# Performance work log

Hardware: AMD Instinct MI355X
Metric: run time of the kernel (lower is better)

## Reference

```python
import jax, jax.numpy as jnp
import numpy as np

ITER_STEPS = 2
NODE_DIM = 512

def _rmv(t, m, value):
    # allennlp.replace_masked_values: keep t where mask nonzero, else value
    return jnp.where(m != 0, t, value)

def setup_inputs() -> dict:
    key = jax.random.key(0)
    ks = jax.random.split(key, 24)
    B, R, C, D, d = 16, 64, 64, 2048, NODE_DIM
    inp = {
        "question_node": jax.random.normal(ks[0], (B, d), jnp.float32),
        "table_row_header_nodes": jax.random.normal(ks[1], (B, R, d), jnp.float32),
        "table_col_header_nodes": jax.random.normal(ks[2], (B, C, d), jnp.float32),
        "table_data_cell_nodes": jax.random.normal(ks[3], (B, D, d), jnp.float32),
        "table_row_header_index_mask": jax.random.randint(ks[4], (B, R), 0, 2, jnp.int32),
        "table_col_header_index_mask": jax.random.randint(ks[5], (B, C), 0, 2, jnp.int32),
        "table_data_cell_index_mask": jax.random.randint(ks[6], (B, D), 0, 2, jnp.int32),
        "same_row_data_cell_relation": jax.random.randint(ks[7], (B, D, D), 0, 2, jnp.int32),
        "same_col_data_cell_relation": jax.random.randint(ks[8], (B, D, D), 0, 2, jnp.int32),
        "data_cell_row_rel": jax.random.randint(ks[9], (B, R, D), 0, 2, jnp.int32),
        "data_cell_col_rel": jax.random.randint(ks[10], (B, C, D), 0, 2, jnp.int32),
        # parameters (Linear(in,out) stores weight [out,in]; y = x @ W.T)
        "w_node": jax.random.normal(ks[11], (1, d), jnp.float32) / np.sqrt(d),
        "w_row_data_cell": jax.random.normal(ks[12], (d, d), jnp.float32) / np.sqrt(d),
        "w_col_data_cell": jax.random.normal(ks[13], (d, d), jnp.float32) / np.sqrt(d),
        "w_data_cell_row": jax.random.normal(ks[14], (d, d), jnp.float32) / np.sqrt(d),
        "w_data_cell_col": jax.random.normal(ks[15], (d, d), jnp.float32) / np.sqrt(d),
        "w_same_row": jax.random.normal(ks[16], (d, d), jnp.float32) / np.sqrt(d),
        "w_same_col": jax.random.normal(ks[17], (d, d), jnp.float32) / np.sqrt(d),
        "w_row_question": jax.random.normal(ks[18], (d, d), jnp.float32) / np.sqrt(d),
        "w_col_question": jax.random.normal(ks[19], (d, d), jnp.float32) / np.sqrt(d),
    }
    return inp


def reference(question_node, table_row_header_nodes, table_col_header_nodes,
              table_data_cell_nodes, table_row_header_index_mask,
              table_col_header_index_mask, table_data_cell_index_mask,
              same_row_data_cell_relation, same_col_data_cell_relation,
              data_cell_row_rel, data_cell_col_rel,
              w_node, w_row_data_cell, w_col_data_cell, w_data_cell_row,
              w_data_cell_col, w_same_row, w_same_col, w_row_question,
              w_col_question):
    rm = table_row_header_index_mask.astype(jnp.float32)   # [B,R]
    cm = table_col_header_index_mask.astype(jnp.float32)   # [B,C]
    dm = table_data_cell_index_mask.astype(jnp.float32)    # [B,D]

    # masked relation graphs (0/1 float)
    rh_dc_graph = data_cell_row_rel.astype(jnp.float32) * (rm[:, :, None] * dm[:, None, :])   # [B,R,D]
    ch_dc_graph = data_cell_col_rel.astype(jnp.float32) * (cm[:, :, None] * dm[:, None, :])   # [B,C,D]
    dc_dc_mask = dm[:, :, None] * dm[:, None, :]
    same_row_graph = same_row_data_cell_relation.astype(jnp.float32) * dc_dc_mask             # [B,D,D]
    same_col_graph = same_col_data_cell_relation.astype(jnp.float32) * dc_dc_mask             # [B,D,D]

    rh_num = rh_dc_graph.sum(-1)                                  # [B,R]
    rh_num = _rmv(rh_num + 1.0, (rh_num >= 1), 1.0)
    ch_num = ch_dc_graph.sum(-1)                                  # [B,C]
    ch_num = _rmv(ch_num + 1.0, (ch_num >= 1), 1.0)
    dc_num = (same_row_graph.sum(-1) + same_col_graph.sum(-1)
              + rh_dc_graph.sum(1) + ch_dc_graph.sum(1))          # [B,D]
    dc_num = _rmv(dc_num, (dc_num >= 1), 1.0)

    rh = table_row_header_nodes
    ch = table_col_header_nodes
    dc = table_data_cell_nodes
    q = question_node

    for _ in range(ITER_STEPS):
        rh_w = jax.nn.sigmoid(rh @ w_node.T)[..., 0]   # [B,R]
        ch_w = jax.nn.sigmoid(ch @ w_node.T)[..., 0]   # [B,C]
        dc_w = jax.nn.sigmoid(dc @ w_node.T)[..., 0]   # [B,D]

        rh_dc_info = dc @ w_row_data_cell.T            # [B,D,d]
        ch_dc_info = dc @ w_col_data_cell.T            # [B,D,d]
        rh_q_info = (q @ w_row_question.T)[:, None, :] * rm[:, :, None]  # [B,R,d]
        ch_q_info = (q @ w_col_question.T)[:, None, :] * cm[:, :, None]  # [B,C,d]
        same_row_info = dc @ w_same_row.T              # [B,D,d]
        same_col_info = dc @ w_same_col.T              # [B,D,d]
        dc_rh_info = rh @ w_data_cell_row.T            # [B,R,d]
        dc_ch_info = ch @ w_data_cell_col.T            # [B,C,d]

        # gated adjacency weights: source-node sigmoid gate masked by graph
        rh_dc_weight = jnp.where(rh_dc_graph != 0, dc_w[:, None, :], 0.0)         # [B,R,D]
        ch_dc_weight = jnp.where(ch_dc_graph != 0, dc_w[:, None, :], 0.0)         # [B,C,D]
        same_row_weight = jnp.where(same_row_graph != 0, dc_w[:, None, :], 0.0)   # [B,D,D]
        same_col_weight = jnp.where(same_col_graph != 0, dc_w[:, None, :], 0.0)   # [B,D,D]
        dc_rh_weight = jnp.where(jnp.swapaxes(rh_dc_graph, 1, 2) != 0, rh_w[:, None, :], 0.0)  # [B,D,R]
        dc_ch_weight = jnp.where(jnp.swapaxes(ch_dc_graph, 1, 2) != 0, ch_w[:, None, :], 0.0)  # [B,D,C]

        rh_dc_agg = jnp.matmul(rh_dc_weight, rh_dc_info)        # [B,R,d]
        ch_dc_agg = jnp.matmul(ch_dc_weight, ch_dc_info)        # [B,C,d]
        same_row_agg = jnp.matmul(same_row_weight, same_row_info)  # [B,D,d]
        same_col_agg = jnp.matmul(same_col_weight, same_col_info)  # [B,D,d]
        dc_rh_agg = jnp.matmul(dc_rh_weight, dc_rh_info)        # [B,D,d]
        dc_ch_agg = jnp.matmul(dc_ch_weight, dc_ch_info)        # [B,D,d]

        agg_rh = (rh_dc_agg + rh_q_info) / rh_num[:, :, None]
        agg_ch = (ch_dc_agg + ch_q_info) / ch_num[:, :, None]
        # NOTE: faithful to source bug: dc_ch_agg appears twice, same_col_agg unused
        agg_dc = (same_row_agg + dc_ch_agg + dc_rh_agg + dc_ch_agg) / dc_num[:, :, None]

        rh = jax.nn.relu(agg_rh)
        ch = jax.nn.relu(agg_ch)
        dc = jax.nn.relu(agg_dc)

    return (rh, ch, dc)
```

## Files before the change

### kernel.cpp

```cpp
#include <hip/hip_runtime.h>
#include <math.h>

#define NB 16
#define NR 64
#define NCOL 64
#define ND 2048
#define DIM 512

typedef __attribute__((ext_vector_type(4))) float f32x4;
typedef __attribute__((ext_vector_type(8))) short bf16x8;
typedef __attribute__((ext_vector_type(8))) unsigned short us8;

#define OFF_RHNUM  0L
#define OFF_CHNUM  1024L
#define OFF_DCNUM  2048L
#define OFF_RHW    34816L
#define OFF_CHW    35840L
#define OFF_QROW   36864L
#define OFF_QCOL   45056L
#define OFF_PRER   53248L
#define OFF_PREC   577536L
#define OFF_INFORC 1101824L
#define OFF_BITS   2150400L
#define OFF_DCS    4247552L
#define OFF_PROJ   21024768L
#define WS_FLOATS  37801984L

__device__ inline void bsplit(float v, unsigned short& h, unsigned short& l) {
    unsigned uv = __float_as_uint(v);
    unsigned hb = (uv + 0x7FFFu + ((uv >> 16) & 1u)) >> 16;
    h = (unsigned short)hb;
    float lo = v - __uint_as_float(hb << 16);
    unsigned lv = __float_as_uint(lo);
    l = (unsigned short)((lv + 0x7FFFu + ((lv >> 16) & 1u)) >> 16);
}

__global__ __launch_bounds__(256) void k_gate_rc(
    const float* __restrict__ rh, const float* __restrict__ ch,
    const int* __restrict__ rm, const int* __restrict__ cm,
    const float* __restrict__ wnode,
    float* __restrict__ rh_w, float* __restrict__ ch_w)
{
    int wave = threadIdx.x >> 6, lane = threadIdx.x & 63;
    int idx = blockIdx.x * 4 + wave;
    const float* xrow; float* outw; int mval;
    if (idx < NB * NR) {
        int b = idx >> 6, r = idx & 63;
        xrow = rh + ((long)b * NR + r) * DIM; mval = rm[b * NR + r]; outw = rh_w + b * NR + r;
    } else {
        int tt = idx - NB * NR; int b = tt >> 6, c = tt & 63;
        xrow = ch + ((long)b * NCOL + c) * DIM; mval = cm[b * NCOL + c]; outw = ch_w + b * NCOL + c;
    }
    const float4* px = (const float4*)xrow;
    const float4* pw = (const float4*)wnode;
    float4 xa = px[lane * 2], xb = px[lane * 2 + 1];
    float4 wa = pw[lane * 2], wb = pw[lane * 2 + 1];
    float s = xa.x * wa.x + xa.y * wa.y + xa.z * wa.z + xa.w * wa.w
            + xb.x * wb.x + xb.y * wb.y + xb.z * wb.z + xb.w * wb.w;
    #pragma unroll
    for (int o = 32; o > 0; o >>= 1) s += __shfl_xor(s, o, 64);
    if (lane == 0) {
        float g = 1.f / (1.f + expf(-s));
        *outw = mval ? g : 0.f;
    }
}

__global__ __launch_bounds__(256) void k_split(
    const float* __restrict__ src, const float* __restrict__ wnode, const int* __restrict__ dmask,
    unsigned short* __restrict__ dhi, unsigned short* __restrict__ dlo)
{
    int wave = threadIdx.x >> 6, lane = threadIdx.x & 63;
    long idx = (long)blockIdx.x * 4 + wave;
    const float* row = src + idx * DIM;
    const float4* px = (const float4*)row;
    const float4* pw = (const float4*)wnode;
    float4 xa = px[lane * 2], xb = px[lane * 2 + 1];
    float4 wa = pw[lane * 2], wb = pw[lane * 2 + 1];
    float s = xa.x * wa.x + xa.y * wa.y + xa.z * wa.z + xa.w * wa.w
            + xb.x * wb.x + xb.y * wb.y + xb.z * wb.z + xb.w * wb.w;
    #pragma unroll
    for (int o = 32; o > 0; o >>= 1) s += __shfl_xor(s, o, 64);
    float g = 1.f / (1.f + expf(-s));
    float sc = (dmask[idx] != 0) ? g : 0.f;
    float v[8] = {sc * xa.x, sc * xa.y, sc * xa.z, sc * xa.w,
                  sc * xb.x, sc * xb.y, sc * xb.z, sc * xb.w};
    us8 ph, pl;
    #pragma unroll
    for (int i = 0; i < 8; i++) {
        unsigned short hh, ll; bsplit(v[i], hh, ll);
        ph[i] = hh; pl[i] = ll;
    }
    *(us8*)(dhi + idx * DIM + lane * 8) = ph;
    *(us8*)(dlo + idx * DIM + lane * 8) = pl;
}

__global__ __launch_bounds__(256) void k_wsplit(
    const float* __restrict__ w, unsigned short* __restrict__ whi, unsigned short* __restrict__ wlo)
{
    long i = ((long)blockIdx.x * 256 + threadIdx.x) * 8;
    float4 a = *(const float4*)(w + i), b4 = *(const float4*)(w + i + 4);
    float v[8] = {a.x, a.y, a.z, a.w, b4.x, b4.y, b4.z, b4.w};
    us8 ph, pl;
    #pragma unroll
    for (int t = 0; t < 8; t++) {
        unsigned short hh, ll; bsplit(v[t], hh, ll);
        ph[t] = hh; pl[t] = ll;
    }
    *(us8*)(whi + i) = ph;
    *(us8*)(wlo + i) = pl;
}

__global__ __launch_bounds__(256) void k_q(
    const float* __restrict__ q, const float* __restrict__ wrq, const float* __restrict__ wcq,
    float* __restrict__ qrow, float* __restrict__ qcol)
{
    int b = blockIdx.z;
    const float* W = blockIdx.y ? wcq : wrq;
    float* out = blockIdx.y ? qcol : qrow;
    int wave = threadIdx.x >> 6, lane = threadIdx.x & 63;
    int n = blockIdx.x * 4 + wave;
    const float4* qp = (const float4*)(q + (long)b * DIM);
    const float4* wp = (const float4*)(W + (long)n * DIM);
    float4 a0 = qp[lane * 2], a1 = qp[lane * 2 + 1];
    float4 w0 = wp[lane * 2], w1 = wp[lane * 2 + 1];
    float s = a0.x * w0.x + a0.y * w0.y + a0.z * w0.z + a0.w * w0.w
            + a1.x * w1.x + a1.y * w1.y + a1.z * w1.z + a1.w * w1.w;
    #pragma unroll
    for (int o = 32; o > 0; o >>= 1) s += __shfl_xor(s, o, 64);
    if (lane == 0) out[(long)b * DIM + n] = s;
}

__global__ __launch_bounds__(256) void k_bits(
    const int* __restrict__ sr, const int* __restrict__ sc, const int* __restrict__ dmask,
    unsigned* __restrict__ bits, float* __restrict__ dcnum)
{
    long bi = blockIdx.x;
    int b = (int)(bi >> 11);
    const int* dmb = dmask + (long)b * ND;
    int dmi = dmb[bi & 2047];
    int wave = threadIdx.x >> 6, lane = threadIdx.x & 63;
    const int* srrow = sr + bi * ND;
    const int* scrow = sc + bi * ND;
    unsigned* brow = bits + bi * 64;
    int cnt = 0;
    for (int rr = 0; rr < 8; rr++) {
        int j = wave * 512 + rr * 64 + lane;
        int dmj = dmb[j] != 0;
        bool p1 = dmi && dmj && (srrow[j] != 0);
        unsigned long long m1 = __ballot(p1);
        bool p2 = dmi && dmj && (scrow[j] != 0);
        unsigned long long m2 = __ballot(p2);
        if (lane == 0) {
            int w0 = wave * 16 + rr * 2;
            brow[w0] = (unsigned)m1; brow[w0 + 1] = (unsigned)(m1 >> 32);
        }
        cnt += __popcll(m1) + __popcll(m2);
    }
    __shared__ int red[4];
    if (lane == 0) red[wave] = cnt;
    __syncthreads();
    if (threadIdx.x == 0) dcnum[bi] = (float)(red[0] + red[1] + red[2] + red[3]);
}

__global__ __launch_bounds__(256) void k_rcnum(
    const int* __restrict__ rel_rd, const int* __restrict__ rel_cd,
    const int* __restrict__ rm, const int* __restrict__ cm, const int* __restrict__ dmask,
    float* __restrict__ rh_num, float* __restrict__ ch_num)
{
    int wave = threadIdx.x >> 6, lane = threadIdx.x & 63;
    long idx = (long)blockIdx.x * 4 + wave;
    const int* row; int mval; float* out; const int* dmb;
    if (idx < NB * NR) {
        int b = (int)(idx >> 6), r = (int)(idx & 63);
        row = rel_rd + ((long)b * NR + r) * ND; mval = rm[b * NR + r];
        out = rh_num + b * NR + r; dmb = dmask + (long)b * ND;
    } else {
        long tt = idx - NB * NR; int b = (int)(tt >> 6), c = (int)(tt & 63);
        row = rel_cd + ((long)b * NCOL + c) * ND; mval = cm[b * NCOL + c];
        out = ch_num + b * NCOL + c; dmb = dmask + (long)b * ND;
    }
    int cnt = 0;
    for (int rr = 0; rr < 32; rr++) {
        int j = rr * 64 + lane;
        cnt += (row[j] != 0 && dmb[j] != 0) ? 1 : 0;
    }
    #pragma unroll
    for (int o = 32; o > 0; o >>= 1) cnt += __shfl_xor(cnt, o, 64);
    if (lane == 0) {
        float s = mval ? (float)cnt : 0.f;
        *out = (s >= 1.f) ? (s + 1.f) : 1.f;
    }
}

__global__ __launch_bounds__(256) void k_dcnum_final(
    const int* __restrict__ rel_rd, const int* __restrict__ rel_cd,
    const int* __restrict__ rm, const int* __restrict__ cm, const int* __restrict__ dmask,
    float* __restrict__ dcnum)
{
    int b = blockIdx.y;
    int j = blockIdx.x * 256 + threadIdx.x;
    const int* rd = rel_rd + (long)b * NR * ND;
    const int* cd = rel_cd + (long)b * NCOL * ND;
    const int* rmb = rm + b * NR;
    const int* cmb = cm + b * NCOL;
    int cnt = 0;
    for (int r = 0; r < NR; r++)  cnt += (rd[(long)r * ND + j] != 0 && rmb[r] != 0) ? 1 : 0;
    for (int c = 0; c < NCOL; c++) cnt += (cd[(long)c * ND + j] != 0 && cmb[c] != 0) ? 1 : 0;
    float add = (dmask[(long)b * ND + j] != 0) ? (float)cnt : 0.f;
    float tv = dcnum[(long)b * ND + j] + add;
    dcnum[(long)b * ND + j] = (tv >= 1.f) ? tv : 1.f;
}

template<int EPI>
__global__ __launch_bounds__(256) void gemm_small(
    const float* __restrict__ A, long sA,
    const float* __restrict__ W,
    float* __restrict__ C, long sC,
    const float* __restrict__ rowscale, float alpha,
    const int* __restrict__ mrow, const float* __restrict__ addvec,
    const float* __restrict__ rownum, int rsb)
{
    int b = blockIdx.z;
    int n0 = blockIdx.x * 64;
    __shared__ float As[32][68], Ws[32][68];
    float acc[4][4] = {};
    int tx = threadIdx.x & 15, ty = threadIdx.x >> 4;
    int lm = threadIdx.x >> 2, lk = (threadIdx.x & 3) * 8;
    const float* Ab = A + (long)b * sA;
    for (int k0 = 0; k0 < DIM; k0 += 32) {
        const float4* pa = (const float4*)(Ab + (long)lm * DIM + k0 + lk);
        float4 va0 = pa[0], va1 = pa[1];
        const float4* pw = (const float4*)(W + (long)(n0 + lm) * DIM + k0 + lk);
        float4 vw0 = pw[0], vw1 = pw[1];
        As[lk + 0][lm] = va0.x; As[lk + 1][lm] = va0.y; As[lk + 2][lm] = va0.z; As[lk + 3][lm] = va0.w;
        As[lk + 4][lm] = va1.x; As[lk + 5][lm] = va1.y; As[lk + 6][lm] = va1.z; As[lk + 7][lm] = va1.w;
        Ws[lk + 0][lm] = vw0.x; Ws[lk + 1][lm] = vw0.y; Ws[lk + 2][lm] = vw0.z; Ws[lk + 3][lm] = vw0.w;
        Ws[lk + 4][lm] = vw1.x; Ws[lk + 5][lm] = vw1.y; Ws[lk + 6][lm] = vw1.z; Ws[lk + 7][lm] = vw1.w;
        __syncthreads();
        #pragma unroll
        for (int kk = 0; kk < 32; kk++) {
            float4 av = *(const float4*)&As[kk][ty * 4];
            float4 wv = *(const float4*)&Ws[kk][tx * 4];
            float a[4] = {av.x, av.y, av.z, av.w};
            float w[4] = {wv.x, wv.y, wv.z, wv.w};
            #pragma unroll
            for (int mi = 0; mi < 4; mi++)
                #pragma unroll
                for (int ni = 0; ni < 4; ni++)
                    acc[mi][ni] += a[mi] * w[ni];
        }
        __syncthreads();
    }
    #pragma unroll
    for (int mi = 0; mi < 4; mi++) {
        int gm = ty * 4 + mi;
        float vals[4];
        if (EPI == 1) {
            float scv = alpha * rowscale[(long)b * rsb + gm];
            #pragma unroll
            for (int ni = 0; ni < 4; ni++) vals[ni] = scv * acc[mi][ni];
        } else {
            float mq = (mrow[(long)b * rsb + gm] != 0) ? 1.f : 0.f;
            float inv = 1.f / rownum[(long)b * rsb + gm];
            #pragma unroll
            for (int ni = 0; ni < 4; ni++) {
                float tv = (acc[mi][ni] + mq * addvec[(long)b * DIM + n0 + tx * 4 + ni]) * inv;
                vals[ni] = fmaxf(tv, 0.f);
            }
        }
        float4 o; o.x = vals[0]; o.y = vals[1]; o.z = vals[2]; o.w = vals[3];
        *(float4*)(C + (long)b * sC + (long)gm * DIM + n0 + tx * 4) = o;
    }
}

__global__ __launch_bounds__(256) void k_proj_mfma(
    const unsigned short* __restrict__ whi, const unsigned short* __restrict__ wlo,
    const unsigned short* __restrict__ dhi, const unsigned short* __restrict__ dlo,
    unsigned short* __restrict__ phi, unsigned short* __restrict__ plo)
{
    int flat = blockIdx.x;
    int tile = (flat & 7) * 128 + (flat >> 3);
    int b = tile >> 6;
    int rem = tile & 63;
    int m0 = (rem >> 4) * 128;
    int n0 = (rem & 15) * 128;

    __shared__ unsigned short Ahi[128 * 64], Alo[128 * 64];
    __shared__ unsigned short Bhi[128 * 64], Blo[128 * 64];

    int tid = threadIdx.x;
    int lane = tid & 63, wid = tid >> 6;
    int wm = wid >> 1, wn = wid & 1;

    int srow = tid >> 1, sseg = tid & 1;

    f32x4 acc[4][4];
    #pragma unroll
    for (int i = 0; i < 4; i++)
        #pragma unroll
        for (int j = 0; j < 4; j++)
            acc[i][j] = (f32x4){0.f, 0.f, 0.f, 0.f};

    for (int k0 = 0; k0 < DIM; k0 += 64) {
        {
            const uint4* ph = (const uint4*)(whi + (long)(m0 + srow) * DIM + k0 + sseg * 32);
            const uint4* pl = (const uint4*)(wlo + (long)(m0 + srow) * DIM + k0 + sseg * 32);
            #pragma unroll
            for (int s = 0; s < 4; s++) {
                int c = (sseg * 4 + s) ^ (srow & 7);
                *(uint4*)((char*)Ahi + srow * 128 + c * 16) = ph[s];
                *(uint4*)((char*)Alo + srow * 128 + c * 16) = pl[s];
            }
        }
        {
            const uint4* ph = (const uint4*)(dhi + ((long)b * ND + n0 + srow) * DIM + k0 + sseg * 32);
            const uint4* pl = (const uint4*)(dlo + ((long)b * ND + n0 + srow) * DIM + k0 + sseg * 32);
            #pragma unroll
            for (int s = 0; s < 4; s++) {
                int c = (sseg * 4 + s) ^ (srow & 7);
                *(uint4*)((char*)Bhi + srow * 128 + c * 16) = ph[s];
                *(uint4*)((char*)Blo + srow * 128 + c * 16) = pl[s];
            }
        }
        __syncthreads();
        #pragma unroll
        for (int ks = 0; ks < 2; ks++) {
            bf16x8 ah[4], al[4], bh[4], bl[4];
            #pragma unroll
            for (int i = 0; i < 4; i++) {
                int rr = wm * 64 + i * 16 + (lane & 15);
                int cc = (ks * 4 + (lane >> 4)) ^ (rr & 7);
                ah[i] = *(bf16x8*)((char*)Ahi + rr * 128 + cc * 16);
                al[i] = *(bf16x8*)((char*)Alo + rr * 128 + cc * 16);
                int nn = wn * 64 + i * 16 + (lane & 15);
                int c2 = (ks * 4 + (lane >> 4)) ^ (nn & 7);
                bh[i] = *(bf16x8*)((char*)Bhi + nn * 128 + c2 * 16);
                bl[i] = *(bf16x8*)((char*)Blo + nn * 128 + c2 * 16);
            }
            #pragma unroll
            for (int mi = 0; mi < 4; mi++)
                #pragma unroll
                for (int ni = 0; ni < 4; ni++) {
                    acc[mi][ni] = __builtin_amdgcn_mfma_f32_16x16x32_bf16(ah[mi], bh[ni], acc[mi][ni], 0, 0, 0);
                    acc[mi][ni] = __builtin_amdgcn_mfma_f32_16x16x32_bf16(ah[mi], bl[ni], acc[mi][ni], 0, 0, 0);
                    acc[mi][ni] = __builtin_amdgcn_mfma_f32_16x16x32_bf16(al[mi], bh[ni], acc[mi][ni], 0, 0, 0);
                }
        }
        __syncthreads();
    }
    #pragma unroll
    for (int mi = 0; mi < 4; mi++) {
        int grow = m0 + wm * 64 + mi * 16 + (lane >> 4) * 4;
        #pragma unroll
        for (int ni = 0; ni < 4; ni++) {
            int gcol = n0 + wn * 64 + ni * 16 + (lane & 15);
            #pragma unroll
            for (int r = 0; r < 4; r++) {
                unsigned short hh, ll; bsplit(acc[mi][ni][r], hh, ll);
                long off = ((long)b * DIM + grow + r) * ND + gcol;
                phi[off] = hh; plo[off] = ll;
            }
        }
    }
}

__global__ __launch_bounds__(256) void k_pre_rc(
    const int* __restrict__ rel_rd, const int* __restrict__ rel_cd,
    const unsigned short* __restrict__ dhi, const unsigned short* __restrict__ dlo,
    const int* __restrict__ rm, const int* __restrict__ cm,
    float* __restrict__ pre_r, float* __restrict__ pre_c)
{
    int b = blockIdx.z, n0 = blockIdx.x * 64;
    const int* rel = blockIdx.y ? rel_cd : rel_rd;
    const int* msk = blockIdx.y ? cm : rm;
    float* outp = blockIdx.y ? pre_c : pre_r;
    __shared__ float As[64][68], Bs[64][68];
    float acc[4][4] = {};
    int tx = threadIdx.x & 15, ty = threadIdx.x >> 4;
    int am = threadIdx.x >> 2, ak = (threadIdx.x & 3) * 16;
    int bj = threadIdx.x >> 2, bseg = threadIdx.x & 3;
    for (int k0 = 0; k0 < ND; k0 += 64) {
        const int4* pa = (const int4*)(rel + ((long)b * 64 + am) * ND + k0 + ak);
        #pragma unroll
        for (int s4 = 0; s4 < 4; s4++) {
            int4 v = pa[s4];
            As[ak + s4 * 4 + 0][am] = v.x ? 1.f : 0.f;
            As[ak + s4 * 4 + 1][am] = v.y ? 1.f : 0.f;
            As[ak + s4 * 4 + 2][am] = v.z ? 1.f : 0.f;
            As[ak + s4 * 4 + 3][am] = v.w ? 1.f : 0.f;
        }
        long sb = ((long)b * ND + k0 + bj) * DIM + n0 + bseg * 16;
        us8 h0 = *(const us8*)(dhi + sb);
        us8 h1 = *(const us8*)(dhi + sb + 8);
        us8 l0 = *(const us8*)(dlo + sb);
        us8 l1 = *(const us8*)(dlo + sb + 8);
        #pragma unroll
        for (int t = 0; t < 8; t++) {
            Bs[bj][bseg * 16 + t] =
                __uint_as_float((unsigned)h0[t] << 16) + __uint_as_float((unsigned)l0[t] << 16);
            Bs[bj][bseg * 16 + 8 + t] =
                __uint_as_float((unsigned)h1[t] << 16) + __uint_as_float((unsigned)l1[t] << 16);
        }
        __syncthreads();
        #pragma unroll 8
        for (int kk = 0; kk < 64; kk++) {
            float4 av = *(const float4*)&As[kk][ty * 4];
            float4 bv = *(const float4*)&Bs[kk][tx * 4];
            float a[4] = {av.x, av.y, av.z, av.w};
            float w[4] = {bv.x, bv.y, bv.z, bv.w};
            #pragma unroll
            for (int mi = 0; mi < 4; mi++)
                #pragma unroll
                for (int ni = 0; ni < 4; ni++)
                    acc[mi][ni] += a[mi] * w[ni];
        }
        __syncthreads();
    }
    #pragma unroll
    for (int mi = 0; mi < 4; mi++) {
        int gm = ty * 4 + mi;
        float scv = (msk[b * 64 + gm] != 0) ? 1.f : 0.f;
        float4 o; o.x = scv * acc[mi][0]; o.y = scv * acc[mi][1]; o.z = scv * acc[mi][2]; o.w = scv * acc[mi][3];
        *(float4*)(outp + ((long)b * 64 + gm) * DIM + n0 + tx * 4) = o;
    }
}

__global__ __launch_bounds__(256) void k_aggdc(
    const int* __restrict__ rel_rd, const int* __restrict__ rel_cd,
    const float* __restrict__ info_rc, const int* __restrict__ dmask,
    float* __restrict__ out)
{
    int b = blockIdx.z, m0 = blockIdx.y * 128, n0 = blockIdx.x * 128;
    __shared__ float As[32][132], Bs[32][132];
    float acc[8][8] = {};
    int tx = threadIdx.x & 15, ty = threadIdx.x >> 4;
    int ak = threadIdx.x >> 3, aj = (threadIdx.x & 7) * 16;
    for (int kt = 0; kt < 4; kt++) {
        const int* rel = (kt < 2) ? rel_rd : rel_cd;
        int krow = (kt & 1) * 32 + ak;
        const int4* pa = (const int4*)(rel + ((long)b * 64 + krow) * ND + m0 + aj);
        #pragma unroll
        for (int s = 0; s < 4; s++) {
            int4 v = pa[s];
            float4 f; f.x = v.x ? 1.f : 0.f; f.y = v.y ? 1.f : 0.f; f.z = v.z ? 1.f : 0.f; f.w = v.w ? 1.f : 0.f;
            *(float4*)&As[ak][aj + s * 4] = f;
        }
        const float4* pb = (const float4*)(info_rc + ((long)b * 128 + kt * 32 + ak) * DIM + n0 + aj);
        #pragma unroll
        for (int s = 0; s < 4; s++) *(float4*)&Bs[ak][aj + s * 4] = pb[s];
        __syncthreads();
        #pragma unroll 4
        for (int kk = 0; kk < 32; kk++) {
            float4 a0 = *(const float4*)&As[kk][ty * 8];
            float4 a1 = *(const float4*)&As[kk][ty * 8 + 4];
            float4 b0 = *(const float4*)&Bs[kk][tx * 8];
            float4 b1 = *(const float4*)&Bs[kk][tx * 8 + 4];
            float a[8] = {a0.x, a0.y, a0.z, a0.w, a1.x, a1.y, a1.z, a1.w};
            float w[8] = {b0.x, b0.y, b0.z, b0.w, b1.x, b1.y, b1.z, b1.w};
            #pragma unroll
            for (int mi = 0; mi < 8; mi++)
                #pragma unroll
                for (int ni = 0; ni < 8; ni++)
                    acc[mi][ni] += a[mi] * w[ni];
        }
        __syncthreads();
    }
    #pragma unroll
    for (int mi = 0; mi < 8; mi++) {
        int gm = m0 + ty * 8 + mi;
        float mq = (dmask[(long)b * ND + gm] != 0) ? 1.f : 0.f;
        float* po = out + ((long)b * ND + gm) * DIM + n0 + tx * 8;
        float4 o0; o0.x = mq * acc[mi][0]; o0.y = mq * acc[mi][1]; o0.z = mq * acc[mi][2]; o0.w = mq * acc[mi][3];
        float4 o1; o1.x = mq * acc[mi][4]; o1.y = mq * acc[mi][5]; o1.z = mq * acc[mi][6]; o1.w = mq * acc[mi][7];
        *(float4*)(po) = o0; *(float4*)(po + 4) = o1;
    }
}

__global__ __launch_bounds__(256) void k_agg_final(
    const unsigned* __restrict__ bits,
    const unsigned short* __restrict__ phi, const unsigned short* __restrict__ plo,
    const float* __restrict__ aggdc, const float* __restrict__ rownum,
    float* __restrict__ out)
{
    int flat = blockIdx.x;
    int tile = (flat & 7) * 128 + (flat >> 3);
    int b = tile >> 6;
    int m0 = ((tile >> 2) & 15) * 128;
    int n0 = (tile & 3) * 128;

    __shared__ unsigned short Aexp[128 * 64];
    __shared__ unsigned short Bhi[128 * 64];
    __shared__ unsigned short Blo[128 * 64];

    int tid = threadIdx.x;
    int lane = tid & 63, wid = tid >> 6;
    int wm = wid >> 1, wn = wid & 1;

    int arow = tid >> 1, awsel = tid & 1;
    const unsigned* abit_base = bits + ((long)b * ND + m0 + arow) * 64 + awsel;

    f32x4 acc[4][4];
    #pragma unroll
    for (int i = 0; i < 4; i++)
        #pragma unroll
        for (int j = 0; j < 4; j++)
            acc[i][j] = (f32x4){0.f, 0.f, 0.f, 0.f};

    for (int k0 = 0; k0 < ND; k0 += 64) {
        #pragma unroll
        for (int u = 0; u < 8; u++) {
            int lin = (u & 3) * 256 + tid;
            int n = lin >> 3, c = lin & 7;
            const unsigned short* src = (u < 4 ? phi : plo)
                + ((long)b * DIM + n0 + n) * ND + k0 + c * 8;
            uint4 v = *(const uint4*)src;
            char* dst = (char*)(u < 4 ? Bhi : Blo) + n * 128 + ((c ^ (n & 7)) * 16);
            *(uint4*)dst = v;
        }
        {
            unsigned w = abit_base[k0 >> 5];
            char* ab = (char*)Aexp + arow * 128;
            #pragma unroll
            for (int c = 0; c < 4; c++) {
                uint4 qv;
                qv.x = (((w >> (c * 8 + 0)) & 1u) ? 0x3F80u : 0u) | (((w >> (c * 8 + 1)) & 1u) ? 0x3F800000u : 0u);
                qv.y = (((w >> (c * 8 + 2)) & 1u) ? 0x3F80u : 0u) | (((w >> (c * 8 + 3)) & 1u) ? 0x3F800000u : 0u);
                qv.z = (((w >> (c * 8 + 4)) & 1u) ? 0x3F80u : 0u) | (((w >> (c * 8 + 5)) & 1u) ? 0x3F800000u : 0u);
                qv.w = (((w >> (c * 8 + 6)) & 1u) ? 0x3F80u : 0u) | (((w >> (c * 8 + 7)) & 1u) ? 0x3F800000u : 0u);
                int chunk = (awsel * 4 + c) ^ (arow & 7);
                *(uint4*)(ab + chunk * 16) = qv;
            }
        }
        __syncthreads();
        #pragma unroll
        for (int ks = 0; ks < 2; ks++) {
            bf16x8 af[4], bh[4], bl[4];
            #pragma unroll
            for (int i = 0; i < 4; i++) {
                int rr = wm * 64 + i * 16 + (lane & 15);
                int cc = (ks * 4 + (lane >> 4)) ^ (rr & 7);
                af[i] = *(bf16x8*)((char*)Aexp + rr * 128 + cc * 16);
                int nn = wn * 64 + i * 16 + (lane & 15);
                int c2 = (ks * 4 + (lane >> 4)) ^ (nn & 7);
                bh[i] = *(bf16x8*)((char*)Bhi + nn * 128 + c2 * 16);
                bl[i] = *(bf16x8*)((char*)Blo + nn * 128 + c2 * 16);
            }
            #pragma unroll
            for (int mi = 0; mi < 4; mi++)
                #pragma unroll
                for (int ni = 0; ni < 4; ni++) {
                    acc[mi][ni] = __builtin_amdgcn_mfma_f32_16x16x32_bf16(af[mi], bh[ni], acc[mi][ni], 0, 0, 0);
                    acc[mi][ni] = __builtin_amdgcn_mfma_f32_16x16x32_bf16(af[mi], bl[ni], acc[mi][ni], 0, 0, 0);
                }
        }
        __syncthreads();
    }
    #pragma unroll
    for (int mi = 0; mi < 4; mi++) {
        int grow = m0 + wm * 64 + mi * 16 + (lane >> 4) * 4;
        float inv[4];
        #pragma unroll
        for (int r = 0; r < 4; r++) inv[r] = 1.f / rownum[(long)b * ND + grow + r];
        #pragma unroll
        for (int ni = 0; ni < 4; ni++) {
            int gcol = n0 + wn * 64 + ni * 16 + (lane & 15);
            #pragma unroll
            for (int r = 0; r < 4; r++) {
                long off = ((long)b * ND + grow + r) * DIM + gcol;
                out[off] = fmaxf((acc[mi][ni][r] + aggdc[off]) * inv[r], 0.f);
            }
        }
    }
}

extern "C" void kernel_launch(void* const* d_in, const int* in_sizes, int n_in,
                              void* d_out, int out_size, void* d_ws, size_t ws_size,
                              hipStream_t stream)
{
    const float* q       = (const float*)d_in[0];
    const float* rh0     = (const float*)d_in[1];
    const float* ch0     = (const float*)d_in[2];
    const float* dc0     = (const float*)d_in[3];
    const int*   rm      = (const int*)d_in[4];
    const int*   cm      = (const int*)d_in[5];
    const int*   dmask   = (const int*)d_in[6];
    const int*   same_row= (const int*)d_in[7];
    const int*   same_col= (const int*)d_in[8];
    const int*   rel_rd  = (const int*)d_in[9];
    const int*   rel_cd  = (const int*)d_in[10];
    const float* wnode   = (const float*)d_in[11];
    const float* w_rdc   = (const float*)d_in[12];
    const float* w_cdc   = (const float*)d_in[13];
    const float* w_dcr   = (const float*)d_in[14];
    const float* w_dcc   = (const float*)d_in[15];
    const float* w_sr    = (const float*)d_in[16];
    const float* w_rq    = (const float*)d_in[18];
    const float* w_cq    = (const float*)d_in[19];

    float* out = (float*)d_out;
    float* rh = out;
    float* ch = out + (long)NB * NR * DIM;
    float* dc = out + (long)NB * NR * DIM * 2;

    if (ws_size < (size_t)WS_FLOATS * 4) return;

    float* ws      = (float*)d_ws;
    float* rh_num  = ws + OFF_RHNUM;
    float* ch_num  = ws + OFF_CHNUM;
    float* dc_num  = ws + OFF_DCNUM;
    float* rh_w    = ws + OFF_RHW;
    float* ch_w    = ws + OFF_CHW;
    float* qrow    = ws + OFF_QROW;
    float* qcol    = ws + OFF_QCOL;
    float* pre_r   = ws + OFF_PRER;
    float* pre_c   = ws + OFF_PREC;
    float* info_rc = ws + OFF_INFORC;
    unsigned* bits = (unsigned*)(ws + OFF_BITS);
    unsigned short* dhi = (unsigned short*)(ws + OFF_DCS);
    unsigned short* dlo = dhi + (size_t)NB * ND * DIM;
    unsigned short* phi = (unsigned short*)(ws + OFF_PROJ);
    unsigned short* plo = phi + (size_t)NB * DIM * ND;
    float* aggdc   = ws + OFF_DCS;
    unsigned short* whi = (unsigned short*)(ws + OFF_PRER);
    unsigned short* wlo = whi + (size_t)DIM * DIM;

    hipMemcpyAsync(rh, rh0, sizeof(float) * (size_t)NB * NR * DIM, hipMemcpyDeviceToDevice, stream);
    hipMemcpyAsync(ch, ch0, sizeof(float) * (size_t)NB * NCOL * DIM, hipMemcpyDeviceToDevice, stream);

    k_bits<<<NB * ND, 256, 0, stream>>>(same_row, same_col, dmask, bits, dc_num);
    k_rcnum<<<512, 256, 0, stream>>>(rel_rd, rel_cd, rm, cm, dmask, rh_num, ch_num);
    k_dcnum_final<<<dim3(ND / 256, NB), 256, 0, stream>>>(rel_rd, rel_cd, rm, cm, dmask, dc_num);
    k_q<<<dim3(128, 2, NB), 256, 0, stream>>>(q, w_rq, w_cq, qrow, qcol);

    for (int it = 0; it < 2; it++) {
        k_gate_rc<<<512, 256, 0, stream>>>(rh, ch, rm, cm, wnode, rh_w, ch_w);
        k_split<<<8192, 256, 0, stream>>>(it == 0 ? dc0 : dc, wnode, dmask, dhi, dlo);
        k_wsplit<<<128, 256, 0, stream>>>(w_sr, whi, wlo);
        gemm_small<1><<<dim3(8, 1, NB), 256, 0, stream>>>(rh, (long)NR * DIM, w_dcr,
            info_rc, 128L * DIM, rh_w, 1.0f, nullptr, nullptr, nullptr, NR);
        gemm_small<1><<<dim3(8, 1, NB), 256, 0, stream>>>(ch, (long)NCOL * DIM, w_dcc,
            info_rc + 64L * DIM, 128L * DIM, ch_w, 2.0f, nullptr, nullptr, nullptr, NCOL);
        k_proj_mfma<<<1024, 256, 0, stream>>>(whi, wlo, dhi, dlo, phi, plo);
        k_pre_rc<<<dim3(8, 2, NB), 256, 0, stream>>>(rel_rd, rel_cd, dhi, dlo, rm, cm, pre_r, pre_c);
        k_aggdc<<<dim3(4, 16, NB), 256, 0, stream>>>(rel_rd, rel_cd, info_rc, dmask, aggdc);
        gemm_small<2><<<dim3(8, 1, NB), 256, 0, stream>>>(pre_r, (long)NR * DIM, w_rdc,
            rh, (long)NR * DIM, nullptr, 1.0f, rm, qrow, rh_num, NR);
        gemm_small<2><<<dim3(8, 1, NB), 256, 0, stream>>>(pre_c, (long)NCOL * DIM, w_cdc,
            ch, (long)NCOL * DIM, nullptr, 1.0f, cm, qcol, ch_num, NCOL);
        k_agg_final<<<1024, 256, 0, stream>>>(bits, phi, plo, aggdc, dc_num, dc);
    }
}
```

Measured before the change: 1.157 ms.

## Move row/col pre-aggregation to bf16 MFMA using transposed split data cells

k_split now stages 16 data-cell rows in shared memory and, besides the row-major hi/lo bf16 split, writes a transposed hi/lo copy so that a new MFMA kernel can compute the rel_rd/rel_cd times data-cell products with bf16 matrix instructions instead of the FP32 scalar tile GEMM. The transposed buffers reuse the projection workspace, so the pre-aggregation is moved ahead of k_proj_mfma, and the split weights now live in the dc output buffer. k_bits is also rewritten to use vectorised int4 loads and bit interleaving. The cost is extra transposed writes in k_split and a changed bit layout that the consumer must match.

New measurement: 1.147 ms. No clear change (-0.8%).

```diff
diff --git a/kernel.cpp b/kernel.cpp
--- a/kernel.cpp
+++ b/kernel.cpp
@@ -35,6 +35,13 @@
     l = (unsigned short)((lv + 0x7FFFu + ((lv >> 16) & 1u)) >> 16);
 }
 
+__device__ inline unsigned spread4(unsigned x) {
+    x = (x | (x << 12)) & 0x000F000Fu;
+    x = (x | (x << 6))  & 0x03030303u;
+    x = (x | (x << 3))  & 0x11111111u;
+    return x;
+}
+
 __global__ __launch_bounds__(256) void k_gate_rc(
     const float* __restrict__ rh, const float* __restrict__ ch,
     const int* __restrict__ rm, const int* __restrict__ cm,
@@ -67,31 +74,65 @@
 
 __global__ __launch_bounds__(256) void k_split(
     const float* __restrict__ src, const float* __restrict__ wnode, const int* __restrict__ dmask,
-    unsigned short* __restrict__ dhi, unsigned short* __restrict__ dlo)
-{
-    int wave = threadIdx.x >> 6, lane = threadIdx.x & 63;
-    long idx = (long)blockIdx.x * 4 + wave;
-    const float* row = src + idx * DIM;
-    const float4* px = (const float4*)row;
-    const float4* pw = (const float4*)wnode;
-    float4 xa = px[lane * 2], xb = px[lane * 2 + 1];
-    float4 wa = pw[lane * 2], wb = pw[lane * 2 + 1];
-    float s = xa.x * wa.x + xa.y * wa.y + xa.z * wa.z + xa.w * wa.w
-            + xb.x * wb.x + xb.y * wb.y + xb.z * wb.z + xb.w * wb.w;
-    #pragma unroll
-    for (int o = 32; o > 0; o >>= 1) s += __shfl_xor(s, o, 64);
-    float g = 1.f / (1.f + expf(-s));
-    float sc = (dmask[idx] != 0) ? g : 0.f;
-    float v[8] = {sc * xa.x, sc * xa.y, sc * xa.z, sc * xa.w,
-                  sc * xb.x, sc * xb.y, sc * xb.z, sc * xb.w};
-    us8 ph, pl;
+    unsigned short* __restrict__ dhi, unsigned short* __restrict__ dlo,
+    unsigned short* __restrict__ thi, unsigned short* __restrict__ tlo)
+{
+    int b = blockIdx.y, j0 = blockIdx.x * 16;
+    __shared__ float X[16 * 512];
+    __shared__ float scs[16];
+    int t = threadIdx.x;
+    int r = t >> 4, u = t & 15;
+    const float* row = src + ((long)b * ND + j0 + r) * DIM;
+    float part = 0.f;
     #pragma unroll
     for (int i = 0; i < 8; i++) {
-        unsigned short hh, ll; bsplit(v[i], hh, ll);
-        ph[i] = hh; pl[i] = ll;
-    }
-    *(us8*)(dhi + idx * DIM + lane * 8) = ph;
-    *(us8*)(dlo + idx * DIM + lane * 8) = pl;
+        int col = i * 64 + u * 4;
+        float4 v = *(const float4*)(row + col);
+        float4 w = *(const float4*)(wnode + col);
+        part += v.x * w.x + v.y * w.y + v.z * w.z + v.w * w.w;
+        *(float4*)&X[r * 512 + (col ^ ((r & 7) * 4))] = v;
+    }
+    part += __shfl_xor(part, 1, 64);
+    part += __shfl_xor(part, 2, 64);
+    part += __shfl_xor(part, 4, 64);
+    part += __shfl_xor(part, 8, 64);
+    if (u == 0) {
+        float g = 1.f / (1.f + expf(-part));
+        scs[r] = (dmask[(long)b * ND + j0 + r] != 0) ? g : 0.f;
+    }
+    __syncthreads();
+    {
+        float s = scs[r];
+        long ob = ((long)b * ND + j0 + r) * DIM + u * 32;
+        #pragma unroll
+        for (int g = 0; g < 4; g++) {
+            us8 ph, pl;
+            #pragma unroll
+            for (int e = 0; e < 8; e++) {
+                int cc = u * 32 + g * 8 + e;
+                float v = X[r * 512 + (cc ^ ((r & 7) * 4))] * s;
+                unsigned short hh, ll; bsplit(v, hh, ll);
+                ph[e] = hh; pl[e] = ll;
+            }
+            *(us8*)(dhi + ob + g * 8) = ph;
+            *(us8*)(dlo + ob + g * 8) = pl;
+        }
+    }
+    #pragma unroll
+    for (int h = 0; h < 2; h++) {
+        int n = t + h * 256;
+        us8 ph0, ph1, pl0, pl1;
+        #pragma unroll
+        for (int rr = 0; rr < 16; rr++) {
+            float v = X[rr * 512 + (n ^ ((rr & 7) * 4))] * scs[rr];
+            unsigned short hh, ll; bsplit(v, hh, ll);
+            if (rr < 8) { ph0[rr] = hh; pl0[rr] = ll; }
+            else        { ph1[rr - 8] = hh; pl1[rr - 8] = ll; }
+        }
+        long ob = ((long)b * DIM + n) * ND + j0;
+        *(us8*)(thi + ob) = ph0; *(us8*)(thi + ob + 8) = ph1;
+        *(us8*)(tlo + ob) = pl0; *(us8*)(tlo + ob + 8) = pl1;
+    }
 }
 
 __global__ __launch_bounds__(256) void k_wsplit(
@@ -136,25 +177,37 @@
 {
     long bi = blockIdx.x;
     int b = (int)(bi >> 11);
-    const int* dmb = dmask + (long)b * ND;
-    int dmi = dmb[bi & 2047];
+    int dmi = dmask[bi];
     int wave = threadIdx.x >> 6, lane = threadIdx.x & 63;
-    const int* srrow = sr + bi * ND;
-    const int* scrow = sc + bi * ND;
+    const int4* sr4 = (const int4*)(sr + bi * ND);
+    const int4* sc4 = (const int4*)(sc + bi * ND);
+    const int4* dm4 = (const int4*)(dmask + (long)b * ND);
     unsigned* brow = bits + bi * 64;
     int cnt = 0;
-    for (int rr = 0; rr < 8; rr++) {
-        int j = wave * 512 + rr * 64 + lane;
-        int dmj = dmb[j] != 0;
-        bool p1 = dmi && dmj && (srrow[j] != 0);
-        unsigned long long m1 = __ballot(p1);
-        bool p2 = dmi && dmj && (scrow[j] != 0);
-        unsigned long long m2 = __ballot(p2);
-        if (lane == 0) {
-            int w0 = wave * 16 + rr * 2;
-            brow[w0] = (unsigned)m1; brow[w0 + 1] = (unsigned)(m1 >> 32);
-        }
-        cnt += __popcll(m1) + __popcll(m2);
+    #pragma unroll
+    for (int h = 0; h < 2; h++) {
+        int vidx = wave * 128 + h * 64 + lane;
+        int4 vs = sr4[vidx];
+        int4 vc = sc4[vidx];
+        int4 vd = dm4[vidx];
+        bool d0 = dmi && vd.x, d1 = dmi && vd.y, d2 = dmi && vd.z, d3 = dmi && vd.w;
+        unsigned long long m0 = __ballot(d0 && vs.x);
+        unsigned long long m1 = __ballot(d1 && vs.y);
+        unsigned long long m2 = __ballot(d2 && vs.z);
+        unsigned long long m3 = __ballot(d3 && vs.w);
+        unsigned long long n0 = __ballot(d0 && vc.x);
+        unsigned long long n1 = __ballot(d1 && vc.y);
+        unsigned long long n2 = __ballot(d2 && vc.z);
+        unsigned long long n3 = __ballot(d3 && vc.w);
+        cnt += __popcll(m0) + __popcll(m1) + __popcll(m2) + __popcll(m3)
+             + __popcll(n0) + __popcll(n1) + __popcll(n2) + __popcll(n3);
+        if (lane < 8) {
+            unsigned w = spread4((unsigned)(m0 >> (8 * lane)) & 0xFFu)
+                       | (spread4((unsigned)(m1 >> (8 * lane)) & 0xFFu) << 1)
+                       | (spread4((unsigned)(m2 >> (8 * lane)) & 0xFFu) << 2)
+                       | (spread4((unsigned)(m3 >> (8 * lane)) & 0xFFu) << 3);
+            brow[wave * 16 + h * 8 + lane] = w;
+        }
     }
     __shared__ int red[4];
     if (lane == 0) red[wave] = cnt;
@@ -273,6 +326,102 @@
     }
 }
 
+__global__ __launch_bounds__(256) void k_pre_rc_mfma(
+    const int* __restrict__ rel_rd, const int* __restrict__ rel_cd,
+    const unsigned short* __restrict__ thi, const unsigned short* __restrict__ tlo,
+    const int* __restrict__ rm, const int* __restrict__ cm,
+    float* __restrict__ pre_r, float* __restrict__ pre_c)
+{
+    int b = blockIdx.y, n0 = blockIdx.x * 64;
+    __shared__ unsigned short Aexp[128 * 64];
+    __shared__ unsigned short Bhi[64 * 64], Blo[64 * 64];
+    int tid = threadIdx.x, lane = tid & 63, wid = tid >> 6;
+    int wm = wid >> 1, wn = wid & 1;
+    int arow = tid >> 1, aseg = tid & 1;
+    const int* relrow = (arow < 64)
+        ? rel_rd + ((long)b * 64 + arow) * ND
+        : rel_cd + ((long)b * 64 + arow - 64) * ND;
+    int bn = tid >> 2, bq = tid & 3;
+    const unsigned short* bsrc_h = thi + ((long)b * DIM + n0 + bn) * ND;
+    const unsigned short* bsrc_l = tlo + ((long)b * DIM + n0 + bn) * ND;
+
+    f32x4 acc[4][2];
+    #pragma unroll
+    for (int i = 0; i < 4; i++)
+        #pragma unroll
+        for (int j = 0; j < 2; j++)
+            acc[i][j] = (f32x4){0.f, 0.f, 0.f, 0.f};
+
+    for (int k0 = 0; k0 < ND; k0 += 64) {
+        {
+            const int4* pa = (const int4*)(relrow + k0 + aseg * 32);
+            #pragma unroll
+            for (int p = 0; p < 4; p++) {
+                int4 v0 = pa[2 * p], v1 = pa[2 * p + 1];
+                uint4 qv;
+                qv.x = (v0.x ? 0x3F80u : 0u) | (v0.y ? 0x3F800000u : 0u);
+                qv.y = (v0.z ? 0x3F80u : 0u) | (v0.w ? 0x3F800000u : 0u);
+                qv.z = (v1.x ? 0x3F80u : 0u) | (v1.y ? 0x3F800000u : 0u);
+                qv.w = (v1.z ? 0x3F80u : 0u) | (v1.w ? 0x3F800000u : 0u);
+                int c = (aseg * 4 + p) ^ (arow & 7);
+                *(uint4*)((char*)Aexp + arow * 128 + c * 16) = qv;
+            }
+        }
+        {
+            const uint4* ph = (const uint4*)(bsrc_h + k0 + bq * 16);
+            const uint4* pl = (const uint4*)(bsrc_l + k0 + bq * 16);
+            #pragma unroll
+            for (int s = 0; s < 2; s++) {
+                int c = (bq * 2 + s) ^ (bn & 7);
+                *(uint4*)((char*)Bhi + bn * 128 + c * 16) = ph[s];
+                *(uint4*)((char*)Blo + bn * 128 + c * 16) = pl[s];
+            }
+        }
+        __syncthreads();
+        #pragma unroll
+        for (int ks = 0; ks < 2; ks++) {
+            bf16x8 af[4], bh[2], bl[2];
+            #pragma unroll
+            for (int i = 0; i < 4; i++) {
+                int rr = wm * 64 + i * 16 + (lane & 15);
+                int cc = (ks * 4 + (lane >> 4)) ^ (rr & 7);
+                af[i] = *(bf16x8*)((char*)Aexp + rr * 128 + cc * 16);
+            }
+            #pragma unroll
+            for (int i = 0; i < 2; i++) {
+                int nn = wn * 32 + i * 16 + (lane & 15);
+                int c2 = (ks * 4 + (lane >> 4)) ^ (nn & 7);
+                bh[i] = *(bf16x8*)((char*)Bhi + nn * 128 + c2 * 16);
+                bl[i] = *(bf16x8*)((char*)Blo + nn * 128 + c2 * 16);
+            }
+            #pragma unroll
+            for (int mi = 0; mi < 4; mi++)
+                #pragma unroll
+                for (int ni = 0; ni < 2; ni++) {
+                    acc[mi][ni] = __builtin_amdgcn_mfma_f32_16x16x32_bf16(af[mi], bh[ni], acc[mi][ni], 0, 0, 0);
+                    acc[mi][ni] = __builtin_amdgcn_mfma_f32_16x16x32_bf16(af[mi], bl[ni], acc[mi][ni], 0, 0, 0);
+                }
+        }
+        __syncthreads();
+    }
+    const int* msk = wm ? cm : rm;
+    float* outp = wm ? pre_c : pre_r;
+    #pragma unroll
+    for (int mi = 0; mi < 4; mi++) {
+        int grow = mi * 16 + (lane >> 4) * 4;
+        #pragma unroll
+        for (int ni = 0; ni < 2; ni++) {
+            int gcol = n0 + wn * 32 + ni * 16 + (lane & 15);
+            #pragma unroll
+            for (int r = 0; r < 4; r++) {
+                int rrow = grow + r;
+                float scv = (msk[b * 64 + rrow] != 0) ? 1.f : 0.f;
+                outp[((long)b * 64 + rrow) * DIM + gcol] = scv * acc[mi][ni][r];
+            }
+        }
+    }
+}
+
 __global__ __launch_bounds__(256) void k_proj_mfma(
     const unsigned short* __restrict__ whi, const unsigned short* __restrict__ wlo,
     const unsigned short* __restrict__ dhi, const unsigned short* __restrict__ dlo,
@@ -361,67 +510,6 @@
                 phi[off] = hh; plo[off] = ll;
             }
         }
-    }
-}
-
-__global__ __launch_bounds__(256) void k_pre_rc(
-    const int* __restrict__ rel_rd, const int* __restrict__ rel_cd,
-    const unsigned short* __restrict__ dhi, const unsigned short* __restrict__ dlo,
-    const int* __restrict__ rm, const int* __restrict__ cm,
-    float* __restrict__ pre_r, float* __restrict__ pre_c)
-{
-    int b = blockIdx.z, n0 = blockIdx.x * 64;
-    const int* rel = blockIdx.y ? rel_cd : rel_rd;
-    const int* msk = blockIdx.y ? cm : rm;
-    float* outp = blockIdx.y ? pre_c : pre_r;
-    __shared__ float As[64][68], Bs[64][68];
-    float acc[4][4] = {};
-    int tx = threadIdx.x & 15, ty = threadIdx.x >> 4;
-    int am = threadIdx.x >> 2, ak = (threadIdx.x & 3) * 16;
-    int bj = threadIdx.x >> 2, bseg = threadIdx.x & 3;
-    for (int k0 = 0; k0 < ND; k0 += 64) {
-        const int4* pa = (const int4*)(rel + ((long)b * 64 + am) * ND + k0 + ak);
-        #pragma unroll
-        for (int s4 = 0; s4 < 4; s4++) {
-            int4 v = pa[s4];
-            As[ak + s4 * 4 + 0][am] = v.x ? 1.f : 0.f;
-            As[ak + s4 * 4 + 1][am] = v.y ? 1.f : 0.f;
-            As[ak + s4 * 4 + 2][am] = v.z ? 1.f : 0.f;
-            As[ak + s4 * 4 + 3][am] = v.w ? 1.f : 0.f;
-        }
-        long sb = ((long)b * ND + k0 + bj) * DIM + n0 + bseg * 16;
-        us8 h0 = *(const us8*)(dhi + sb);
-        us8 h1 = *(const us8*)(dhi + sb + 8);
-        us8 l0 = *(const us8*)(dlo + sb);
-        us8 l1 = *(const us8*)(dlo + sb + 8);
-        #pragma unroll
-        for (int t = 0; t < 8; t++) {
-            Bs[bj][bseg * 16 + t] =
-                __uint_as_float((unsigned)h0[t] << 16) + __uint_as_float((unsigned)l0[t] << 16);
-            Bs[bj][bseg * 16 + 8 + t] =
-                __uint_as_float((unsigned)h1[t] << 16) + __uint_as_float((unsigned)l1[t] << 16);
-        }
-        __syncthreads();
-        #pragma unroll 8
-        for (int kk = 0; kk < 64; kk++) {
-            float4 av = *(const float4*)&As[kk][ty * 4];
-            float4 bv = *(const float4*)&Bs[kk][tx * 4];
-            float a[4] = {av.x, av.y, av.z, av.w};
-            float w[4] = {bv.x, bv.y, bv.z, bv.w};
-            #pragma unroll
-            for (int mi = 0; mi < 4; mi++)
-                #pragma unroll
-                for (int ni = 0; ni < 4; ni++)
-                    acc[mi][ni] += a[mi] * w[ni];
-        }
-        __syncthreads();
-    }
-    #pragma unroll
-    for (int mi = 0; mi < 4; mi++) {
-        int gm = ty * 4 + mi;
-        float scv = (msk[b * 64 + gm] != 0) ? 1.f : 0.f;
-        float4 o; o.x = scv * acc[mi][0]; o.y = scv * acc[mi][1]; o.z = scv * acc[mi][2]; o.w = scv * acc[mi][3];
-        *(float4*)(outp + ((long)b * 64 + gm) * DIM + n0 + tx * 4) = o;
     }
 }
 
@@ -618,10 +706,12 @@
     unsigned* bits = (unsigned*)(ws + OFF_BITS);
     unsigned short* dhi = (unsigned short*)(ws + OFF_DCS);
     unsigned short* dlo = dhi + (size_t)NB * ND * DIM;
+    unsigned short* thi = (unsigned short*)(ws + OFF_PROJ);
+    unsigned short* tlo = thi + (size_t)NB * DIM * ND;
     unsigned short* phi = (unsigned short*)(ws + OFF_PROJ);
     unsigned short* plo = phi + (size_t)NB * DIM * ND;
     float* aggdc   = ws + OFF_DCS;
-    unsigned short* whi = (unsigned short*)(ws + OFF_PRER);
+    unsigned short* whi = (unsigned short*)dc;
     unsigned short* wlo = whi + (size_t)DIM * DIM;
 
     hipMemcpyAsync(rh, rh0, sizeof(float) * (size_t)NB * NR * DIM, hipMemcpyDeviceToDevice, stream);
@@ -634,14 +724,14 @@
 
     for (int it = 0; it < 2; it++) {
         k_gate_rc<<<512, 256, 0, stream>>>(rh, ch, rm, cm, wnode, rh_w, ch_w);
-        k_split<<<8192, 256, 0, stream>>>(it == 0 ? dc0 : dc, wnode, dmask, dhi, dlo);
+        k_split<<<dim3(128, NB), 256, 0, stream>>>(it == 0 ? dc0 : dc, wnode, dmask, dhi, dlo, thi, tlo);
         k_wsplit<<<128, 256, 0, stream>>>(w_sr, whi, wlo);
         gemm_small<1><<<dim3(8, 1, NB), 256, 0, stream>>>(rh, (long)NR * DIM, w_dcr,
             info_rc, 128L * DIM, rh_w, 1.0f, nullptr, nullptr, nullptr, NR);
         gemm_small<1><<<dim3(8, 1, NB), 256, 0, stream>>>(ch, (long)NCOL * DIM, w_dcc,
             info_rc + 64L * DIM, 128L * DIM, ch_w, 2.0f, nullptr, nullptr, nullptr, NCOL);
+        k_pre_rc_mfma<<<dim3(8, NB), 256, 0, stream>>>(rel_rd, rel_cd, thi, tlo, rm, cm, pre_r, pre_c);
         k_proj_mfma<<<1024, 256, 0, stream>>>(whi, wlo, dhi, dlo, phi, plo);
-        k_pre_rc<<<dim3(8, 2, NB), 256, 0, stream>>>(rel_rd, rel_cd, dhi, dlo, rm, cm, pre_r, pre_c);
         k_aggdc<<<dim3(4, 16, NB), 256, 0, stream>>>(rel_rd, rel_cd, info_rc, dmask, aggdc);
         gemm_small<2><<<dim3(8, 1, NB), 256, 0, stream>>>(pre_r, (long)NR * DIM, w_rdc,
             rh, (long)NR * DIM, nullptr, 1.0f, rm, qrow, rh_num, NR);
```
